# Kernel optimization log

Measured on AMD Instinct MI355X. Metric: run time of the kernel, lower is better.

The kernel has to match this reference:

```python
import jax, jax.numpy as jnp
import numpy as np

B, S, HID = 4, 2048, 1024
E, K, H = 8, 2, 8          # num_experts, topk, num_heads
DK = HID // H              # head_qk_dim = 128
DV = HID // H              # head_v_dim = 128
CAP = int(S * 1.0)         # capacity_len = int((S*K)/K * capacity)
CHUNK = 64
EPS = 1e-5


def setup_inputs() -> dict:
    key = jax.random.key(0)
    ks = jax.random.split(key, 12)
    std = 0.02  # ~ xavier_uniform with gain 2**-2.5
    return {
        "x": jax.random.normal(ks[0], (B, S, HID), jnp.float32),
        "gate_w": jax.random.normal(ks[1], (E, HID), jnp.float32) * std,
        "q_w": jax.random.normal(ks[2], (HID, HID), jnp.float32) * std,
        "k_w": jax.random.normal(ks[3], (E, HID, HID), jnp.float32) * std,
        "v_w": jax.random.normal(ks[4], (E, HID, HID), jnp.float32) * std,
        "fmq1_w": jax.random.normal(ks[5], (DK, DK), jnp.float32) * std,
        "fmq2_w": jax.random.normal(ks[6], (DK, DK), jnp.float32) * std,
        "fmk1_w": jax.random.normal(ks[7], (DK, DK), jnp.float32) * std,
        "fmk2_w": jax.random.normal(ks[8], (DK, DK), jnp.float32) * std,
        "norm_w": jnp.ones((DV,), jnp.float32),
        "o_w": jax.random.normal(ks[9], (HID, HID), jnp.float32) * std,
    }


def chunk_linear_attn(q, k, v):
    # q,k: (Bt, T, H, DK); v: (Bt, T, H, DV). Causal linear attention, chunked.
    Bt, T, Hh, Dk = q.shape
    Dv = v.shape[-1]
    nc = T // CHUNK
    q = q * (Dk ** -0.5)
    qc = q.reshape(Bt, nc, CHUNK, Hh, Dk).transpose(1, 0, 2, 3, 4)
    kc = k.reshape(Bt, nc, CHUNK, Hh, Dk).transpose(1, 0, 2, 3, 4)
    vc = v.reshape(Bt, nc, CHUNK, Hh, Dv).transpose(1, 0, 2, 3, 4)
    causal = jnp.tril(jnp.ones((CHUNK, CHUNK), q.dtype))
    def step(Sst, qkv):
        qb, kb, vb = qkv  # (Bt, CHUNK, H, D)
        attn = jnp.einsum('bihd,bjhd->bhij', qb, kb) * causal
        intra = jnp.einsum('bhij,bjhe->bihe', attn, vb)
        inter = jnp.einsum('bihd,bhde->bihe', qb, Sst)
        Sst = Sst + jnp.einsum('bjhd,bjhe->bhde', kb, vb)
        return Sst, intra + inter
    S0 = jnp.zeros((Bt, Hh, Dk, Dv), q.dtype)
    _, o = jax.lax.scan(step, S0, (qc, kc, vc))
    return o.transpose(1, 0, 2, 3, 4).reshape(Bt, T, Hh, Dv)


def _forward(x, gate_w, q_w, k_w, v_w, fmq1_w, fmq2_w, fmk1_w, fmk2_w, norm_w, o_w):
    b, s0, d = x.shape
    # ---- routing ----
    logits = jnp.einsum('bsd,ed->bse', x, gate_w)
    scores = jax.nn.softmax(logits.astype(jnp.float32), axis=-1)
    rw, sel = jax.lax.top_k(scores, K)                 # (b, s0, K)
    rw = (rw / rw.sum(-1, keepdims=True)).astype(x.dtype)
    routing_mask = jax.nn.one_hot(sel, E, dtype=jnp.int32).sum(2)  # (b, s0, E)
    # ---- transform: sort-by-(batch,expert), capacity gather ----
    s = s0 * K
    x_rep = jnp.repeat(x, K, axis=1).reshape(b * s, d)  # repeat_interleave over seq
    sel_flat = sel.reshape(b * s).astype(jnp.int32)
    batch_idx = jnp.repeat(jnp.arange(b, dtype=jnp.int32), s)
    combined = batch_idx * E + sel_flat
    sorted_indices = jnp.argsort(combined)              # stable in jax
    x_sorted = x_rep[sorted_indices]
    tokens = routing_mask.sum(axis=1)                   # (b, E) tokens per group
    flat_off = (jnp.cumsum(tokens, axis=1) + (jnp.arange(b, dtype=jnp.int32) * s)[:, None]).reshape(-1)
    starts = jnp.concatenate([jnp.zeros((1,), flat_off.dtype), flat_off[:-1]])
    idx = starts[:, None] + jnp.arange(CAP, dtype=flat_off.dtype)[None, :]
    shift = jnp.maximum(tokens.reshape(-1) - CAP, 0)    # keep last CAP tokens
    tidx = idx + shift[:, None]                         # (b*E, CAP)
    dmask = tidx < flat_off[:, None]
    tidx = jnp.where(dmask, tidx, 0)
    xe = x_sorted[tidx.reshape(-1)].reshape(b * E, CAP, d) * dmask[..., None].astype(x.dtype)
    xe = xe.reshape(b, E, CAP, d).transpose(1, 0, 2, 3)  # (E, b, CAP, d)
    # ---- projections + Hadamard feature maps ----
    q = jnp.einsum('ebtc,kc->ebtk', xe, q_w).reshape(E, b, CAP, H, DK)
    k = jnp.einsum('ebtc,ekc->ebtk', xe, k_w).reshape(E, b, CAP, H, DK)
    v = jnp.einsum('ebtc,ekc->ebtk', xe, v_w).reshape(E, b, CAP, H, DV)
    q = jnp.einsum('...d,kd->...k', q, fmq1_w) * jnp.einsum('...d,kd->...k', q, fmq2_w)
    k = jnp.einsum('...d,kd->...k', k, fmk1_w) * jnp.einsum('...d,kd->...k', k, fmk2_w)
    # ---- causal chunked linear attention per (expert, batch) slot ----
    o = chunk_linear_attn(q.reshape(E * b, CAP, H, DK),
                          k.reshape(E * b, CAP, H, DK),
                          v.reshape(E * b, CAP, H, DV))
    # ---- reconstruct: scatter-add back, undo sort, weighted topk combine ----
    oflat = o.reshape(E, b, CAP, H, DV).transpose(1, 0, 2, 3, 4).reshape(b * E * CAP, H, DV)
    oflat = oflat * dmask.reshape(-1)[:, None, None].astype(o.dtype)
    res = jnp.zeros((b * s, H, DV), o.dtype).at[tidx.reshape(-1)].add(oflat)
    inv = jnp.argsort(sorted_indices)
    restored = res[inv].reshape(b, s0, K, H, DV)
    out = (restored * rw[..., None, None]).sum(axis=2)   # (b, s0, H, DV)
    # RMSNorm over head_v_dim, merge heads, output proj
    out = out * jax.lax.rsqrt(jnp.mean(out * out, axis=-1, keepdims=True) + EPS) * norm_w
    out = out.reshape(b, s0, H * DV)
    return jnp.einsum('bsv,dv->bsd', out, o_w)


def reference(x, gate_w, q_w, k_w, v_w, fmq1_w, fmq2_w, fmk1_w, fmk2_w, norm_w, o_w):
    return _forward(x, gate_w, q_w, k_w, v_w, fmq1_w, fmq2_w, fmk1_w, fmk2_w, norm_w, o_w)
```

## Files before the change

### kernel.cpp

```cpp
#include <hip/hip_runtime.h>
#include <stdint.h>

typedef unsigned short u16;
typedef unsigned int   u32;
typedef __attribute__((ext_vector_type(4))) float f32x4;
typedef __attribute__((ext_vector_type(4))) u32   u32x4;
typedef __attribute__((ext_vector_type(8))) __bf16 bf16x8;

#define MFMA16(a,b,c) __builtin_amdgcn_mfma_f32_16x16x32_bf16((a),(b),(c),0,0,0)

#define QSCALE 0.08838834764831845f
#define RMAX   20480

__device__ __forceinline__ float bf2f(u16 x){ u32 u=((u32)x)<<16; float f; __builtin_memcpy(&f,&u,4); return f; }
__device__ __forceinline__ u16 f2bf(float f){ u32 u; __builtin_memcpy(&u,&f,4); u = u + 0x7FFFu + ((u>>16)&1u); return (u16)(u>>16); }
__device__ __forceinline__ u32 pack2(float a, float b){ return (u32)f2bf(a) | ((u32)f2bf(b)<<16); }

__device__ __forceinline__ void gl_lds(const u16* g, u16* l){
  __builtin_amdgcn_global_load_lds(
      (const __attribute__((address_space(1))) void*)g,
      (__attribute__((address_space(3))) void*)l, 16, 0, 0);
}

#define TSW(row, oct) ((row)*72 + ((((oct) ^ (((row)>>3)&7)))<<3))


__device__ __forceinline__ void cvt_body(const float* __restrict__ s, u16* __restrict__ d,
                                         long n8, int lb, int nb){
  long idx = (long)lb*256 + threadIdx.x;
  long stride = (long)nb*256;
  for (long i=idx; i<n8; i+=stride){
    const float* p = s + i*8;
    f32x4 a = *(const f32x4*)p;
    f32x4 b = *(const f32x4*)(p+4);
    u32x4 o;
    o[0]=pack2(a[0],a[1]); o[1]=pack2(a[2],a[3]); o[2]=pack2(b[0],b[1]); o[3]=pack2(b[2],b[3]);
    *(u32x4*)(d + i*8) = o;
  }
}

__device__ __forceinline__ void route_body(const float* __restrict__ x, const float* __restrict__ gw,
  int* __restrict__ sel, float* __restrict__ rw, u16* __restrict__ xb, int lb)
{
  int w = threadIdx.x>>6, lane = threadIdx.x&63;
  int tok = lb*4 + w;
  const float* xr = x + (size_t)tok*1024 + lane*16;
  f32x4 xv[4];
  #pragma unroll
  for (int q=0;q<4;q++) xv[q] = *(const f32x4*)(xr + q*4);
  {
    u16* xrow = xb + (size_t)tok*1024 + lane*16;
    u32x4 o0, o1;
    o0[0]=pack2(xv[0][0],xv[0][1]); o0[1]=pack2(xv[0][2],xv[0][3]);
    o0[2]=pack2(xv[1][0],xv[1][1]); o0[3]=pack2(xv[1][2],xv[1][3]);
    o1[0]=pack2(xv[2][0],xv[2][1]); o1[1]=pack2(xv[2][2],xv[2][3]);
    o1[2]=pack2(xv[3][0],xv[3][1]); o1[3]=pack2(xv[3][2],xv[3][3]);
    *(u32x4*)xrow     = o0;
    *(u32x4*)(xrow+8) = o1;
  }
  float part[8];
  #pragma unroll
  for (int e=0;e<8;e++){
    const float* g = gw + e*1024 + lane*16;
    float s = 0.f;
    #pragma unroll
    for (int q=0;q<4;q++){
      f32x4 gv = *(const f32x4*)(g + q*4);
      s += xv[q][0]*gv[0] + xv[q][1]*gv[1] + xv[q][2]*gv[2] + xv[q][3]*gv[3];
    }
    part[e]=s;
  }
  #pragma unroll
  for (int e=0;e<8;e++){
    float v = part[e];
    #pragma unroll
    for (int off=32; off>0; off>>=1) v += __shfl_xor(v, off, 64);
    part[e]=v;
  }
  if (lane==0){
    int i0=0; float m0=part[0];
    #pragma unroll
    for (int e=1;e<8;e++) if (part[e]>m0){ m0=part[e]; i0=e; }
    int i1=0; float m1=-3.4e38f;
    #pragma unroll
    for (int e=0;e<8;e++) if (e!=i0 && part[e]>m1){ m1=part[e]; i1=e; }
    sel[tok] = i0 | (i1<<8);
    float e1 = expf(m1-m0);
    float inv = 1.f/(1.f+e1);
    rw[tok*2+0] = inv;
    rw[tok*2+1] = e1*inv;
  }
}

__device__ __forceinline__ void prep_body(
  const float* __restrict__ q_w, const float* __restrict__ k_w,
  const float* __restrict__ fmq1, const float* __restrict__ fmq2,
  const float* __restrict__ fmk1, const float* __restrict__ fmk2,
  u16* __restrict__ wA, u16* __restrict__ wB, int l, u16* shmem)
{
  int gi = l>>3;
  int c0 = (l&7)*128;
  const float* fm; const float* ws; u16* wd;
  if (gi < 8)      { int h=gi;    fm=fmq1; ws=q_w + (size_t)h*131072; wd=wA + (size_t)h*262144; }
  else if (gi < 16){ int h=gi-8;  fm=fmq2; ws=q_w + (size_t)h*131072; wd=wA + (size_t)h*262144 + 131072; }
  else if (gi < 80){ int t=gi-16, e=t>>3, h=t&7; fm=fmk1; ws=k_w + (size_t)(e*8+h)*131072; wd=wB + (size_t)e*2097152 + (size_t)h*262144; }
  else             { int t=gi-80, e=t>>3, h=t&7; fm=fmk2; ws=k_w + (size_t)(e*8+h)*131072; wd=wB + (size_t)e*2097152 + (size_t)h*262144 + 131072; }
  u16* Af = shmem;
  u16* Bf = shmem + 128*136;
  int tid = threadIdx.x;
  for (int i=tid; i<4096; i+=256){
    int row = i>>5, col = (i&31)*4;
    f32x4 v = *(const f32x4*)&fm[row*128 + col];
    u16* dp = &Af[row*136 + col];
    *(u32*)dp     = pack2(v[0],v[1]);
    *(u32*)(dp+2) = pack2(v[2],v[3]);
  }
  for (int i=tid; i<4096; i+=256){
    int dd = i>>5, cq = (i&31)*4;
    f32x4 v = *(const f32x4*)&ws[(size_t)dd*1024 + c0 + cq];
    #pragma unroll
    for (int j=0;j<4;j++){
      int c = cq+j;
      Bf[c*136 + (dd ^ (((c>>2)&3)<<3))] = f2bf(v[j]);
    }
  }
  __syncthreads();
  int lane=tid&63, w=tid>>6, wr=w>>1, wc=w&1, lc=lane&15, lr=lane>>4;
  const f32x4 Z4 = {0.f,0.f,0.f,0.f};
  f32x4 acc[4][4];
  #pragma unroll
  for (int i=0;i<4;i++){
    #pragma unroll
    for (int j=0;j<4;j++) acc[i][j]=Z4;
  }
  #pragma unroll
  for (int kk=0; kk<4; ++kk){
    bf16x8 a[4], b[4];
    #pragma unroll
    for (int mi=0;mi<4;mi++)
      a[mi] = *(const bf16x8*)&Af[(wr*64+mi*16+lc)*136 + kk*32 + lr*8];
    #pragma unroll
    for (int ni=0;ni<4;ni++){
      int c = wc*64+ni*16+lc;
      b[ni] = *(const bf16x8*)&Bf[c*136 + ((kk*32 + lr*8) ^ (((c>>2)&3)<<3))];
    }
    #pragma unroll
    for (int mi=0;mi<4;mi++){
      #pragma unroll
      for (int ni=0;ni<4;ni++)
        acc[mi][ni] = MFMA16(a[mi], b[ni], acc[mi][ni]);
    }
  }
  int r0=lr*4;
  #pragma unroll
  for (int mi=0;mi<4;mi++){
    #pragma unroll
    for (int ni=0;ni<4;ni++){
      int col = c0 + wc*64 + ni*16 + lc;
      #pragma unroll
      for (int r=0;r<4;r++){
        int row = wr*64 + mi*16 + r0 + r;
        wd[(size_t)row*1024 + col] = f2bf(acc[mi][ni][r]);
      }
    }
  }
}

__global__ __launch_bounds__(256) void k_pre(
  const float* __restrict__ x, const float* __restrict__ gw,
  int* __restrict__ sel, float* __restrict__ rw,
  const float* __restrict__ q_w, const float* __restrict__ k_w,
  const float* __restrict__ fmq1, const float* __restrict__ fmq2,
  const float* __restrict__ fmk1, const float* __restrict__ fmk2,
  u16* __restrict__ wA, u16* __restrict__ wB, u16* __restrict__ xb,
  const float* __restrict__ v_w, u16* __restrict__ wVb)
{
  __shared__ __align__(16) u16 shmem[2*128*136];
  int bid = blockIdx.x;
  if (bid < 2048)      route_body(x, gw, sel, rw, xb, bid);
  else if (bid < 3200) prep_body(q_w, k_w, fmq1, fmq2, fmk1, fmk2, wA, wB, bid-2048, shmem);
  else                 cvt_body(v_w, wVb, 1048576L, bid-3200, 256);
}

__global__ __launch_bounds__(256) void k_cvtO(const float* __restrict__ o_w, u16* __restrict__ wOb){
  cvt_body(o_w, wOb, 131072L, blockIdx.x, 32);
}

__global__ __launch_bounds__(256) void k_count(const int* __restrict__ sel,
  int* __restrict__ slot_of, int* __restrict__ src_of, int* __restrict__ meta)
{
  int g = blockIdx.x, b = g>>3, e = g&7;
  int tid = threadIdx.x;
  __shared__ int cn[256];
  unsigned char ex[16];
  int cnt=0;
  #pragma unroll
  for (int i=0;i<16;i++){
    int t = tid*16+i;
    int sv = sel[b*2048 + (t>>1)];
    int ee = (t&1) ? ((sv>>8)&255) : (sv&255);
    ex[i]=(unsigned char)ee;
    cnt += (ee==e);
  }
  cn[tid]=cnt;
  __syncthreads();
  for (int off=1; off<256; off<<=1){
    int v = (tid>=off) ? cn[tid-off] : 0;
    __syncthreads();
    cn[tid] += v;
    __syncthreads();
  }
  int total = cn[255];
  int run = cn[tid]-cnt;
  int shift = total>2048 ? total-2048 : 0;
  #pragma unroll
  for (int i=0;i<16;i++){
    int t = tid*16+i;
    if (ex[i]==e){
      int j = run - shift;
      run++;
      slot_of[b*4096 + t] = (j>=0)? j : -1;
      if (j>=0) src_of[g*2048 + j] = t;
    }
  }
  if (tid==0) meta[g]=total;
}

__global__ void k_bases(int* meta){
  if (threadIdx.x || blockIdx.x) return;
  int basev=0, t=0;
  meta[96]=0;
  for (int g=0; g<32; ++g){
    int n = meta[g];
    int nact = n<2048 ? n : 2048;
    int npad = (nact+127)&~127;
    meta[32+g]=nact;
    meta[64+g]=npad;
    meta[129+g]=(nact+63)>>6;
    for (int i=0;i<(npad>>7);++i) meta[192+t++]=g;
    basev += npad;
    meta[97+g]=basev;
  }
  meta[161]=basev;
}

__global__ __launch_bounds__(256) void k_gather(const u16* __restrict__ xb,
  const int* __restrict__ src_of, const int* __restrict__ meta, u16* __restrict__ xg,
  int* __restrict__ tokmap)
{
  int g = blockIdx.y, jb = blockIdx.x;
  int npad = meta[64+g];
  if (jb*64 >= npad) return;
  int nact = meta[32+g], base = meta[96+g];
  int tid = threadIdx.x;
  int j = jb*64 + (tid>>2);
  int quart = tid&3;
  int src = (j<nact) ? src_of[g*2048+j] : -1;
  int token = (src>=0) ? ((g>>3)*2048 + (src>>1)) : 0;
  if (quart==0) tokmap[base+j] = token;
  u16* orow = xg + ((size_t)(base+j))*1024 + quart*256;
  if (src>=0){
    const u16* xr = xb + (size_t)token*1024 + quart*256;
    #pragma unroll
    for (int i=0;i<256;i+=8) *(u32x4*)(orow+i) = *(const u32x4*)(xr+i);
  } else {
    u32x4 z = {0,0,0,0};
    #pragma unroll
    for (int i=0;i<256;i+=8) *(u32x4*)(orow+i)=z;
  }
}

__global__ __launch_bounds__(512) void k_gemmQKV(const u16* __restrict__ xb, const u16* __restrict__ xg,
  const u16* __restrict__ wA, const u16* __restrict__ wB, const u16* __restrict__ wVb,
  u16* __restrict__ qh, u16* __restrict__ kh, u16* __restrict__ vv, const int* __restrict__ meta)
{
  int bid = blockIdx.x;
  int role, tm, tn;
  const u16 *A, *Wp; u16* outB;
  if (bid < 512){
    role=0; int l=bid, xcd=l&7, jj=l>>3, jd=jj>>3;
    tm=xcd*8+jd; tn=jj&7;
    A=xb; Wp=wA + (size_t)tn*262144; outB=qh;
  } else if (bid < 1792){
    role=1; int l=bid-512, xcd=l&7, jj=l>>3, jd=jj>>3;
    tm=xcd*20+jd; tn=jj&7;
    if (tm*128 >= meta[161]) return;
    A=xg; Wp=wB + (size_t)(meta[192+tm]&7)*2097152 + (size_t)tn*262144; outB=kh;
  } else {
    role=2; int l=bid-1792, xcd=l&7, jj=l>>3, jd=jj>>2;
    tm=xcd*20+jd; tn=jj&3;
    if (tm*128 >= meta[161]) return;
    A=xg; Wp=wVb + (size_t)(meta[192+tm]&7)*1048576 + (size_t)tn*262144; outB=vv;
  }

  __shared__ __align__(16) u16 smem[73728];

  int tid=threadIdx.x, lane=tid&63;
  int w=tid>>6, wr=w>>2, wc=w&3, lc=lane&15, lr=lane>>4;
  int swz = lc&7;
  const f32x4 Z4 = {0.f,0.f,0.f,0.f};
  f32x4 acc[4][4];
  #pragma unroll
  for(int i=0;i<4;i++){
    #pragma unroll
    for(int j2=0;j2<4;j2++) acc[i][j2]=Z4;
  }
  size_t lanoff = (size_t)(tid>>3)*1024 + (size_t)(((tid&7)^((tid>>3)&7))*8);
  const u16* Ag = A  + (size_t)tm*131072 + lanoff;
  const u16* Bg = Wp + lanoff;
  int lo = tid*8;

  #define STAGEF(ao, bo, kt) { \
    const u16* ga = Ag + (kt)*64; const u16* gb = Bg + (kt)*64; \
    gl_lds(ga,                 &smem[(ao) + lo]); \
    gl_lds(ga + (size_t)65536, &smem[(ao) + 4096 + lo]); \
    gl_lds(gb,                  &smem[(bo) + lo]); \
    gl_lds(gb + (size_t)65536,  &smem[(bo) + 4096 + lo]); \
    gl_lds(gb + (size_t)131072, &smem[(bo) + 8192 + lo]); \
    gl_lds(gb + (size_t)196608, &smem[(bo) + 12288 + lo]); }

  STAGEF(0, 24576, 0);
  STAGEF(8192, 40960, 1);
  int cur = 0;
  for (int kt=0; kt<16; ++kt){
    if (kt<15) asm volatile("s_waitcnt vmcnt(6)" ::: "memory");
    else       asm volatile("s_waitcnt vmcnt(0)" ::: "memory");
    __builtin_amdgcn_s_barrier();
    if (kt<14){
      int nid = kt+2; nid -= (nid/3)*3;
      STAGEF(nid*8192, 24576+nid*16384, kt+2);
    }
    int ao = cur*8192, bo = 24576 + cur*16384;
    __builtin_amdgcn_s_setprio(1);
    #pragma unroll
    for (int kk=0; kk<2; ++kk){
      bf16x8 a[4], b[4];
      #pragma unroll
      for (int mi=0;mi<4;mi++){
        int row = wr*64+mi*16+lc;
        a[mi] = *(const bf16x8*)&smem[ao + row*64 + (((kk*4+lr)^swz)<<3)];
      }
      #pragma unroll
      for (int ni=0;ni<4;ni++){
        int row = wc*64+ni*16+lc;
        b[ni] = *(const bf16x8*)&smem[bo + row*64 + (((kk*4+lr)^swz)<<3)];
      }
      #pragma unroll
      for (int mi=0;mi<4;mi++){
        #pragma unroll
        for (int ni=0;ni<4;ni++)
          acc[mi][ni] = MFMA16(a[mi], b[ni], acc[mi][ni]);
      }
    }
    __builtin_amdgcn_s_setprio(0);
    cur = (cur==2)?0:cur+1;
  }
  __syncthreads();
  if (role < 2){
    if (wc >= 2){
      #pragma unroll
      for (int mi=0;mi<4;mi++){
        #pragma unroll
        for (int ni=0;ni<4;ni++){
          int col = (wc-2)*64 + ni*16 + lc;
          #pragma unroll
          for (int r=0;r<4;r++)
            ((float*)smem)[(wr*64+mi*16+lr*4+r)*129 + col] = acc[mi][ni][r];
        }
      }
    }
    __syncthreads();
    if (wc < 2){
      float scl = (role==0) ? QSCALE : 1.0f;
      #pragma unroll
      for (int mi=0;mi<4;mi++){
        #pragma unroll
        for (int ni=0;ni<4;ni++){
          int col = wc*64 + ni*16 + lc;
          #pragma unroll
          for (int r=0;r<4;r++){
            int row = wr*64+mi*16+lr*4+r;
            float v = acc[mi][ni][r] * ((float*)smem)[row*129 + col] * scl;
            outB[(size_t)(tm*128+row)*1024 + tn*128 + col] = f2bf(v);
          }
        }
      }
    }
  } else {
    #pragma unroll
    for (int mi=0;mi<4;mi++){
      #pragma unroll
      for (int ni=0;ni<4;ni++){
        int col = tn*256 + wc*64 + ni*16 + lc;
        #pragma unroll
        for (int r=0;r<4;r++){
          int row = tm*128 + wr*64 + mi*16 + lr*4 + r;
          outB[(size_t)row*1024 + col] = f2bf(acc[mi][ni][r]);
        }
      }
    }
  }
  #undef STAGEF
}

__global__ __launch_bounds__(512) void k_gemmO(const u16* __restrict__ A, const u16* __restrict__ W,
  float* __restrict__ outF)
{
  int tnN = gridDim.x;
  int bid = blockIdx.y*tnN + blockIdx.x;
  int chunk = gridDim.y >> 3;
  int xcd = bid & 7, j = bid >> 3;
  int jd = j / tnN;
  int tm = xcd*chunk + jd;
  int tn = j - jd*tnN;

  __shared__ __align__(16) u16 smem[73728];

  int tid=threadIdx.x, lane=tid&63;
  int w=tid>>6, wr=w>>2, wc=w&3, lc=lane&15, lr=lane>>4;
  int swz = lc&7;
  const f32x4 Z4 = {0.f,0.f,0.f,0.f};
  f32x4 acc[4][4];
  #pragma unroll
  for(int i=0;i<4;i++){
    #pragma unroll
    for(int j2=0;j2<4;j2++) acc[i][j2]=Z4;
  }
  size_t lanoff = (size_t)(tid>>3)*1024 + (size_t)(((tid&7)^((tid>>3)&7))*8);
  const u16* Ag = A + (size_t)tm*131072 + lanoff;
  const u16* Bg = W + (size_t)tn*262144 + lanoff;
  int lo = tid*8;

  #define STAGEO(ao, bo, kt) { \
    const u16* ga = Ag + (kt)*64; const u16* gb = Bg + (kt)*64; \
    gl_lds(ga,                 &smem[(ao) + lo]); \
    gl_lds(ga + (size_t)65536, &smem[(ao) + 4096 + lo]); \
    gl_lds(gb,                  &smem[(bo) + lo]); \
    gl_lds(gb + (size_t)65536,  &smem[(bo) + 4096 + lo]); \
    gl_lds(gb + (size_t)131072, &smem[(bo) + 8192 + lo]); \
    gl_lds(gb + (size_t)196608, &smem[(bo) + 12288 + lo]); }

  STAGEO(0, 24576, 0);
  STAGEO(8192, 40960, 1);
  int cur = 0;
  for (int kt=0; kt<16; ++kt){
    if (kt<15) asm volatile("s_waitcnt vmcnt(6)" ::: "memory");
    else       asm volatile("s_waitcnt vmcnt(0)" ::: "memory");
    __builtin_amdgcn_s_barrier();
    if (kt<14){
      int nid = kt+2; nid -= (nid/3)*3;
      STAGEO(nid*8192, 24576+nid*16384, kt+2);
    }
    int ao = cur*8192, bo = 24576 + cur*16384;
    __builtin_amdgcn_s_setprio(1);
    #pragma unroll
    for (int kk=0; kk<2; ++kk){
      bf16x8 a[4], b[4];
      #pragma unroll
      for (int mi=0;mi<4;mi++){
        int row = wr*64+mi*16+lc;
        a[mi] = *(const bf16x8*)&smem[ao + row*64 + (((kk*4+lr)^swz)<<3)];
      }
      #pragma unroll
      for (int ni=0;ni<4;ni++){
        int row = wc*64+ni*16+lc;
        b[ni] = *(const bf16x8*)&smem[bo + row*64 + (((kk*4+lr)^swz)<<3)];
      }
      #pragma unroll
      for (int mi=0;mi<4;mi++){
        #pragma unroll
        for (int ni=0;ni<4;ni++)
          acc[mi][ni] = MFMA16(a[mi], b[ni], acc[mi][ni]);
      }
    }
    __builtin_amdgcn_s_setprio(0);
    cur = (cur==2)?0:cur+1;
  }
  #pragma unroll
  for (int mi=0;mi<4;mi++){
    #pragma unroll
    for (int ni=0;ni<4;ni++){
      int col = tn*256 + wc*64 + ni*16 + lc;
      #pragma unroll
      for (int r=0;r<4;r++){
        int row = tm*128 + wr*64 + mi*16 + lr*4 + r;
        outF[(size_t)row*1024 + col] = acc[mi][ni][r];
      }
    }
  }
  #undef STAGEO
}

__global__ __launch_bounds__(256,1) void k_attn(const u16* __restrict__ qv, const u16* __restrict__ kv,
  const u16* __restrict__ vv, u16* __restrict__ o, const int* __restrict__ meta,
  const int* __restrict__ tokmap)
{
  int g = blockIdx.x>>3, h = blockIdx.x&7;
  int nch = meta[129+g];
  if (nch==0) return;
  int base = meta[96+g];
  __shared__ __align__(16) u16 Qs[64*136];
  __shared__ __align__(16) u16 Ks[64*136];
  __shared__ __align__(16) u16 KTs[128*72];
  __shared__ __align__(16) u16 VTs[128*72];
  __shared__ __align__(16) u16 Ts[2*128*136];
  __shared__ __align__(16) u16 Ps[64*72];
  int tid=threadIdx.x, w=tid>>6, lane=tid&63;
  int wr=w>>1, wc=w&1;
  int lr=lane>>4, lc=lane&15;
  {
    u32x4 z={0,0,0,0};
    for (int i=tid; i<128*136/8; i+=256) *(u32x4*)&Ts[i*8]=z;
  }
  const f32x4 Z4 = {0.f,0.f,0.f,0.f};
  f32x4 accT[4][4];
  #pragma unroll
  for (int i=0;i<4;i++){
    #pragma unroll
    for (int j=0;j<4;j++) accT[i][j]=Z4;
  }
  __syncthreads();
  const u16* kb = kv + (size_t)base*1024 + h*128;
  const u16* vb = vv + (size_t)base*1024 + h*128;
  u16* ob = o + (size_t)base*1024 + h*128;
  int tso = 0;

  for (int c=0; c<nch; ++c){
    #pragma unroll
    for (int it=0; it<4; ++it){
      int id = tid + it*256;
      int row = id>>4, kc = id&15;
      int tok = tokmap[base + c*64 + row];
      *(u32x4*)&Qs[row*136 + kc*8] = *(const u32x4*)(qv + (size_t)tok*1024 + h*128 + kc*8);
      *(u32x4*)&Ks[row*136 + kc*8] = *(const u32x4*)(kb + (size_t)(c*64+row)*1024 + kc*8);
    }
    #pragma unroll
    for (int it=0; it<4; ++it){
      int id = tid + it*256;
      int j = id>>4, dg = id&15;
      int col = (((j>>3) ^ (dg&7))<<3) + (j&7);
      u32x4 kx = *(const u32x4*)(kb + (size_t)(c*64+j)*1024 + dg*8);
      u32x4 vx = *(const u32x4*)(vb + (size_t)(c*64+j)*1024 + dg*8);
      #pragma unroll
      for (int t=0;t<4;t++){
        KTs[(dg*8+t*2  )*72 + col] = (u16)(kx[t]&0xffff);
        KTs[(dg*8+t*2+1)*72 + col] = (u16)(kx[t]>>16);
        VTs[(dg*8+t*2  )*72 + col] = (u16)(vx[t]&0xffff);
        VTs[(dg*8+t*2+1)*72 + col] = (u16)(vx[t]>>16);
      }
    }
    __syncthreads();
    bf16x8 qf[2][4];
    #pragma unroll
    for (int ti=0; ti<2; ++ti){
      #pragma unroll
      for (int ks=0; ks<4; ++ks)
        qf[ti][ks] = *(const bf16x8*)&Qs[(wr*32+ti*16+lc)*136 + ks*32 + lr*8];
    }
    f32x4 accO[2][4];
    #pragma unroll
    for (int i=0;i<2;i++){
      #pragma unroll
      for (int j=0;j<4;j++) accO[i][j]=Z4;
    }
    #pragma unroll
    for (int ks=0; ks<4; ++ks){
      bf16x8 bt[4];
      #pragma unroll
      for (int te=0; te<4; ++te)
        bt[te] = *(const bf16x8*)&Ts[tso + (wc*64+te*16+lc)*136 + ks*32 + lr*8];
      #pragma unroll
      for (int ti=0; ti<2; ++ti){
        #pragma unroll
        for (int te=0; te<4; ++te)
          accO[ti][te] = MFMA16(qf[ti][ks], bt[te], accO[ti][te]);
      }
    }
    f32x4 accP[2][2];
    #pragma unroll
    for (int i=0;i<2;i++){
      #pragma unroll
      for (int j=0;j<2;j++) accP[i][j]=Z4;
    }
    #pragma unroll
    for (int ks=0; ks<4; ++ks){
      bf16x8 bk[2];
      #pragma unroll
      for (int tj=0; tj<2; ++tj)
        bk[tj] = *(const bf16x8*)&Ks[(wc*32+tj*16+lc)*136 + ks*32 + lr*8];
      #pragma unroll
      for (int ti=0; ti<2; ++ti){
        #pragma unroll
        for (int tj=0; tj<2; ++tj)
          accP[ti][tj] = MFMA16(qf[ti][ks], bk[tj], accP[ti][tj]);
      }
    }
    #pragma unroll
    for (int ti=0; ti<2; ++ti){
      #pragma unroll
      for (int tj=0; tj<2; ++tj){
        #pragma unroll
        for (int r=0;r<4;r++){
          int i = wr*32+ti*16+lr*4+r;
          int j = wc*32+tj*16+lc;
          Ps[i*72 + j] = f2bf( (j<=i) ? accP[ti][tj][r] : 0.f );
        }
      }
    }
    __syncthreads();
    #pragma unroll
    for (int ks=0; ks<2; ++ks){
      bf16x8 ap[2], bv[4];
      #pragma unroll
      for (int ti=0; ti<2; ++ti)
        ap[ti] = *(const bf16x8*)&Ps[(wr*32+ti*16+lc)*72 + ks*32 + lr*8];
      #pragma unroll
      for (int te=0; te<4; ++te)
        bv[te] = *(const bf16x8*)&VTs[TSW(wc*64+te*16+lc, ks*4+lr)];
      #pragma unroll
      for (int ti=0; ti<2; ++ti){
        #pragma unroll
        for (int te=0; te<4; ++te)
          accO[ti][te] = MFMA16(ap[ti], bv[te], accO[ti][te]);
      }
    }
    #pragma unroll
    for (int ks=0; ks<2; ++ks){
      bf16x8 av[4], bk2[4];
      #pragma unroll
      for (int te=0; te<4; ++te)
        av[te] = *(const bf16x8*)&VTs[TSW(wr*64+te*16+lc, ks*4+lr)];
      #pragma unroll
      for (int td=0; td<4; ++td)
        bk2[td] = *(const bf16x8*)&KTs[TSW(wc*64+td*16+lc, ks*4+lr)];
      #pragma unroll
      for (int te=0; te<4; ++te){
        #pragma unroll
        for (int td=0; td<4; ++td)
          accT[te][td] = MFMA16(av[te], bk2[td], accT[te][td]);
      }
    }
    int tsn = tso ^ (128*136);
    #pragma unroll
    for (int te=0; te<4; ++te){
      #pragma unroll
      for (int td=0; td<4; ++td){
        int dk = wc*64+td*16+lc;
        #pragma unroll
        for (int r=0;r<4;r++){
          int erow = wr*64+te*16+lr*4+r;
          Ts[tsn + erow*136 + dk] = f2bf(accT[te][td][r]);
        }
      }
    }
    #pragma unroll
    for (int ti=0; ti<2; ++ti){
      #pragma unroll
      for (int te=0; te<4; ++te){
        int ecol = wc*64+te*16+lc;
        #pragma unroll
        for (int r=0;r<4;r++){
          int i = wr*32+ti*16+lr*4+r;
          ob[(size_t)(c*64+i)*1024 + ecol] = f2bf(accO[ti][te][r]);
        }
      }
    }
    __syncthreads();
    tso = tsn;
  }
}

__global__ __launch_bounds__(256) void k_comb(const u16* __restrict__ o, const int* __restrict__ sel,
  const float* __restrict__ rw, const int* __restrict__ slot_of, const int* __restrict__ meta,
  const float* __restrict__ nw, u16* __restrict__ fin)
{
  int w=threadIdx.x>>6, lane=threadIdx.x&63;
  int tok = blockIdx.x*4 + w;
  int b = tok>>11;
  int sv = sel[tok];
  float acc[16];
  #pragma unroll
  for (int i=0;i<16;i++) acc[i]=0.f;
  #pragma unroll
  for (int kk=0; kk<2; ++kk){
    int e = kk ? ((sv>>8)&255) : (sv&255);
    int j = slot_of[tok*2 + kk];
    if (j < 0) continue;
    float wgt = rw[tok*2+kk];
    int row = meta[96 + b*8 + e] + j;
    const u16* orow = o + (size_t)row*1024 + lane*16;
    #pragma unroll
    for (int q=0;q<2;q++){
      u32x4 v = *(const u32x4*)(orow + q*8);
      #pragma unroll
      for (int t=0;t<4;t++){
        acc[q*8+t*2]   += wgt * bf2f((u16)(v[t]&0xffff));
        acc[q*8+t*2+1] += wgt * bf2f((u16)(v[t]>>16));
      }
    }
  }
  float ssq=0.f;
  #pragma unroll
  for (int i=0;i<16;i++) ssq += acc[i]*acc[i];
  ssq += __shfl_xor(ssq,1,64);
  ssq += __shfl_xor(ssq,2,64);
  ssq += __shfl_xor(ssq,4,64);
  float sc = rsqrtf(ssq*(1.f/128.f) + 1e-5f);
  int cbase = (lane&7)*16;
  u32x4 o0, o1;
  #pragma unroll
  for (int t=0;t<4;t++)
    o0[t] = pack2(acc[2*t]*sc*nw[cbase+2*t], acc[2*t+1]*sc*nw[cbase+2*t+1]);
  #pragma unroll
  for (int t=0;t<4;t++)
    o1[t] = pack2(acc[8+2*t]*sc*nw[cbase+8+2*t], acc[8+2*t+1]*sc*nw[cbase+8+2*t+1]);
  u16* fp = fin + (size_t)tok*1024 + lane*16;
  *(u32x4*)fp     = o0;
  *(u32x4*)(fp+8) = o1;
}

extern "C" void kernel_launch(void* const* d_in, const int* in_sizes, int n_in,
                              void* d_out, int out_size, void* d_ws, size_t ws_size,
                              hipStream_t stream)
{
  (void)in_sizes; (void)n_in;
  const float* x     = (const float*)d_in[0];
  const float* gate  = (const float*)d_in[1];
  const float* q_w   = (const float*)d_in[2];
  const float* k_w   = (const float*)d_in[3];
  const float* v_w   = (const float*)d_in[4];
  const float* fmq1  = (const float*)d_in[5];
  const float* fmq2  = (const float*)d_in[6];
  const float* fmk1  = (const float*)d_in[7];
  const float* fmk2  = (const float*)d_in[8];
  const float* norm_w= (const float*)d_in[9];
  const float* o_w   = (const float*)d_in[10];
  float* out = (float*)d_out;

  uint8_t* ws = (uint8_t*)d_ws;
  size_t off = 0;
  auto alloc = [&](size_t bytes)->void*{ void* p = ws + off; off += (bytes + 255) & ~(size_t)255; return p; };
  int*   meta = (int*)alloc(4096);
  int*   sel  = (int*)alloc(8192*4);
  float* rwb  = (float*)alloc(8192*2*4);
  int*   slot = (int*)alloc(16384*4);
  int*   srcf = (int*)alloc((size_t)32*2048*4);
  int*   tokm = (int*)alloc((size_t)RMAX*4);
  u16* wA = (u16*)alloc((size_t)2097152*2);
  u16* wB = (u16*)alloc((size_t)8*2097152*2);
  u16* xb  = (u16*)alloc((size_t)8192*1024*2);
  u16* xg  = (u16*)alloc((size_t)RMAX*1024*2);
  u16* qh  = (u16*)alloc((size_t)8192*1024*2);
  u16* kh  = (u16*)alloc((size_t)RMAX*1024*2);
  u16* vv  = (u16*)alloc((size_t)RMAX*1024*2);
  if (off > ws_size){
    hipMemsetAsync(d_out, 0x7F, (size_t)out_size*4, stream);
    return;
  }
  u16* wVb = (u16*)d_out;
  u16* ob  = xg;
  u16* fin = qh;
  u16* wOb = wA;

  k_pre<<<3456,256,0,stream>>>(x, gate, sel, rwb, q_w, k_w, fmq1, fmq2, fmk1, fmk2, wA, wB, xb, v_w, wVb);
  k_count<<<32,256,0,stream>>>(sel, slot, srcf, meta);
  k_bases<<<1,64,0,stream>>>(meta);
  k_gather<<<dim3(32,32),256,0,stream>>>(xb, srcf, meta, xg, tokm);
  k_gemmQKV<<<2432,512,0,stream>>>(xb, xg, wA, wB, wVb, qh, kh, vv, meta);
  k_cvtO<<<32,256,0,stream>>>(o_w, wOb);
  k_attn<<<256,256,0,stream>>>(qh, kh, vv, ob, meta, tokm);
  k_comb<<<2048,256,0,stream>>>(ob, sel, rwb, slot, meta, norm_w, fin);
  k_gemmO<<<dim3(4,64),512,0,stream>>>(fin, wOb, out);
}
```

Measured before the change: 416.7 us.

## Enlarge QKV GEMM M-tile to 256 rows with 4-stage K32 LDS pipeline

The fused Q/K/V GEMM now computes 256x256 (or 256x128 for the Q/K elementwise-product roles) output tiles instead of 128-row tiles. It uses a K step of 32 with a 4-deep global-to-LDS ring, a new XOR swizzle, and split barriers that interleave loads with MFMAs. Expert row groups are padded to 256 instead of 128, so the maximum row buffer and the tile-to-expert map change to match. The larger wB weight buffer moves into the output buffer and wVb moves into the workspace. The goal is higher arithmetic intensity and fewer blocks and weight reloads. The costs are more padding waste, higher register pressure from 128 accumulator floats per thread, and an occupancy hint that may force spills.

New measurement: 459.5 us. 1.1x slower.

```diff
diff --git a/kernel.cpp b/kernel.cpp
--- a/kernel.cpp
+++ b/kernel.cpp
@@ -10,7 +10,7 @@
 #define MFMA16(a,b,c) __builtin_amdgcn_mfma_f32_16x16x32_bf16((a),(b),(c),0,0,0)
 
 #define QSCALE 0.08838834764831845f
-#define RMAX   20480
+#define RMAX   24576
 
 __device__ __forceinline__ float bf2f(u16 x){ u32 u=((u32)x)<<16; float f; __builtin_memcpy(&f,&u,4); return f; }
 __device__ __forceinline__ u16 f2bf(float f){ u32 u; __builtin_memcpy(&u,&f,4); u = u + 0x7FFFu + ((u>>16)&1u); return (u16)(u>>16); }
@@ -233,11 +233,11 @@
   for (int g=0; g<32; ++g){
     int n = meta[g];
     int nact = n<2048 ? n : 2048;
-    int npad = (nact+127)&~127;
+    int npad = (nact+255)&~255;
     meta[32+g]=nact;
     meta[64+g]=npad;
     meta[129+g]=(nact+63)>>6;
-    for (int i=0;i<(npad>>7);++i) meta[192+t++]=g;
+    for (int i=0;i<(npad>>8);++i) meta[192+t++]=g;
     basev += npad;
     meta[97+g]=basev;
   }
@@ -270,102 +270,107 @@
   }
 }
 
-__global__ __launch_bounds__(512) void k_gemmQKV(const u16* __restrict__ xb, const u16* __restrict__ xg,
+__global__ __launch_bounds__(512,2) void k_gemmQKV(const u16* __restrict__ xb, const u16* __restrict__ xg,
   const u16* __restrict__ wA, const u16* __restrict__ wB, const u16* __restrict__ wVb,
   u16* __restrict__ qh, u16* __restrict__ kh, u16* __restrict__ vv, const int* __restrict__ meta)
 {
   int bid = blockIdx.x;
   int role, tm, tn;
   const u16 *A, *Wp; u16* outB;
-  if (bid < 512){
-    role=0; int l=bid, xcd=l&7, jj=l>>3, jd=jj>>3;
-    tm=xcd*8+jd; tn=jj&7;
+  if (bid < 256){
+    role=0; int l=bid, xcd=l&7, jj=l>>3;
+    int jd=jj>>3; tm=xcd*4+jd; tn=jj&7;
     A=xb; Wp=wA + (size_t)tn*262144; outB=qh;
-  } else if (bid < 1792){
-    role=1; int l=bid-512, xcd=l&7, jj=l>>3, jd=jj>>3;
-    tm=xcd*20+jd; tn=jj&7;
-    if (tm*128 >= meta[161]) return;
+  } else if (bid < 1024){
+    role=1; int l=bid-256, xcd=l&7, jj=l>>3;
+    int jd=jj>>3; tm=xcd*12+jd; tn=jj&7;
+    if (tm*256 >= meta[161]) return;
     A=xg; Wp=wB + (size_t)(meta[192+tm]&7)*2097152 + (size_t)tn*262144; outB=kh;
   } else {
-    role=2; int l=bid-1792, xcd=l&7, jj=l>>3, jd=jj>>2;
-    tm=xcd*20+jd; tn=jj&3;
-    if (tm*128 >= meta[161]) return;
+    role=2; int l=bid-1024, xcd=l&7, jj=l>>3;
+    int jd=jj>>2; tm=xcd*12+jd; tn=jj&3;
+    if (tm*256 >= meta[161]) return;
     A=xg; Wp=wVb + (size_t)(meta[192+tm]&7)*1048576 + (size_t)tn*262144; outB=vv;
   }
 
-  __shared__ __align__(16) u16 smem[73728];
+  __shared__ __align__(16) u16 smem[65536];
 
   int tid=threadIdx.x, lane=tid&63;
   int w=tid>>6, wr=w>>2, wc=w&3, lc=lane&15, lr=lane>>4;
-  int swz = lc&7;
+  int szl=(lc^(lc>>2))&3;
   const f32x4 Z4 = {0.f,0.f,0.f,0.f};
-  f32x4 acc[4][4];
-  #pragma unroll
-  for(int i=0;i<4;i++){
+  f32x4 acc[8][4];
+  #pragma unroll
+  for(int i=0;i<8;i++){
     #pragma unroll
     for(int j2=0;j2<4;j2++) acc[i][j2]=Z4;
   }
-  size_t lanoff = (size_t)(tid>>3)*1024 + (size_t)(((tid&7)^((tid>>3)&7))*8);
-  const u16* Ag = A  + (size_t)tm*131072 + lanoff;
-  const u16* Bg = Wp + lanoff;
-  int lo = tid*8;
-
-  #define STAGEF(ao, bo, kt) { \
-    const u16* ga = Ag + (kt)*64; const u16* gb = Bg + (kt)*64; \
-    gl_lds(ga,                 &smem[(ao) + lo]); \
-    gl_lds(ga + (size_t)65536, &smem[(ao) + 4096 + lo]); \
-    gl_lds(gb,                  &smem[(bo) + lo]); \
-    gl_lds(gb + (size_t)65536,  &smem[(bo) + 4096 + lo]); \
-    gl_lds(gb + (size_t)131072, &smem[(bo) + 8192 + lo]); \
-    gl_lds(gb + (size_t)196608, &smem[(bo) + 12288 + lo]); }
-
-  STAGEF(0, 24576, 0);
-  STAGEF(8192, 40960, 1);
-  int cur = 0;
-  for (int kt=0; kt<16; ++kt){
-    if (kt<15) asm volatile("s_waitcnt vmcnt(6)" ::: "memory");
-    else       asm volatile("s_waitcnt vmcnt(0)" ::: "memory");
-    __builtin_amdgcn_s_barrier();
-    if (kt<14){
-      int nid = kt+2; nid -= (nid/3)*3;
-      STAGEF(nid*8192, 24576+nid*16384, kt+2);
-    }
-    int ao = cur*8192, bo = 24576 + cur*16384;
-    __builtin_amdgcn_s_setprio(1);
-    #pragma unroll
-    for (int kk=0; kk<2; ++kk){
-      bf16x8 a[4], b[4];
-      #pragma unroll
-      for (int mi=0;mi<4;mi++){
-        int row = wr*64+mi*16+lc;
-        a[mi] = *(const bf16x8*)&smem[ao + row*64 + (((kk*4+lr)^swz)<<3)];
-      }
-      #pragma unroll
-      for (int ni=0;ni<4;ni++){
-        int row = wc*64+ni*16+lc;
-        b[ni] = *(const bf16x8*)&smem[bo + row*64 + (((kk*4+lr)^swz)<<3)];
-      }
-      #pragma unroll
-      for (int mi=0;mi<4;mi++){
-        #pragma unroll
-        for (int ni=0;ni<4;ni++)
-          acc[mi][ni] = MFMA16(a[mi], b[ni], acc[mi][ni]);
-      }
-    }
-    __builtin_amdgcn_s_setprio(0);
-    cur = (cur==2)?0:cur+1;
-  }
+  const u16* Ag = A + (size_t)tm*262144;
+  const u16* Bg = Wp;
+  int grow = tid>>2;
+  int gch  = (((tid&3)^((grow^(grow>>2))&3)))*8;
+  int lch  = (tid&3)*8;
+
+  #define STG(t_, h_) { \
+    const u16* gs = ((h_)&2) ? Bg : Ag; \
+    int rb = ((h_)&1)*128; \
+    gl_lds(gs + (size_t)(rb+grow)*1024 + (size_t)(t_)*32 + gch, \
+           smem + (((t_)&3)<<14) + (((h_)&2)?8192:0) + (rb+grow)*32 + lch); \
+  }
+
+  STG(0,0); STG(0,1); STG(0,2); STG(0,3);
+  STG(1,0); STG(1,1); STG(1,2); STG(1,3);
+  asm volatile("s_waitcnt vmcnt(4)" ::: "memory");
+  __builtin_amdgcn_s_barrier();
+
+  for (int t=0; t<32; ++t){
+    int abase=(t&3)<<14, bbase=abase+8192;
+    bf16x8 a[8];
+    #pragma unroll
+    for (int q=0;q<2;++q){
+      if (q==0){
+        #pragma unroll
+        for (int mi=0;mi<8;mi++){
+          int arow = wr*128+mi*16+lc;
+          a[mi] = *(const bf16x8*)&smem[abase + arow*32 + ((lr^szl)<<3)];
+        }
+      }
+      bf16x8 b[2];
+      #pragma unroll
+      for (int nj=0;nj<2;nj++){
+        int brow = wc*64+(q*2+nj)*16+lc;
+        b[nj] = *(const bf16x8*)&smem[bbase + brow*32 + ((lr^szl)<<3)];
+      }
+      if (t<30){ STG(t+2, q*2); STG(t+2, q*2+1); }
+      __builtin_amdgcn_s_barrier();
+      __builtin_amdgcn_s_setprio(1);
+      #pragma unroll
+      for (int mi=0;mi<8;mi++){
+        #pragma unroll
+        for (int nj=0;nj<2;nj++)
+          acc[mi][q*2+nj] = MFMA16(a[mi], b[nj], acc[mi][q*2+nj]);
+      }
+      __builtin_amdgcn_s_setprio(0);
+      if (q==1){
+        if (t<30)      asm volatile("s_waitcnt vmcnt(4)" ::: "memory");
+        else if (t==30) asm volatile("s_waitcnt vmcnt(0)" ::: "memory");
+      }
+      __builtin_amdgcn_s_barrier();
+    }
+  }
+  #undef STG
+
   __syncthreads();
   if (role < 2){
     if (wc >= 2){
       #pragma unroll
-      for (int mi=0;mi<4;mi++){
+      for (int mi=0;mi<8;mi++){
         #pragma unroll
         for (int ni=0;ni<4;ni++){
           int col = (wc-2)*64 + ni*16 + lc;
           #pragma unroll
           for (int r=0;r<4;r++)
-            ((float*)smem)[(wr*64+mi*16+lr*4+r)*129 + col] = acc[mi][ni][r];
+            ((float*)smem)[(wr*128+mi*16+lr*4+r)*128 + col] = acc[mi][ni][r];
         }
       }
     }
@@ -373,34 +378,33 @@
     if (wc < 2){
       float scl = (role==0) ? QSCALE : 1.0f;
       #pragma unroll
-      for (int mi=0;mi<4;mi++){
+      for (int mi=0;mi<8;mi++){
         #pragma unroll
         for (int ni=0;ni<4;ni++){
           int col = wc*64 + ni*16 + lc;
           #pragma unroll
           for (int r=0;r<4;r++){
-            int row = wr*64+mi*16+lr*4+r;
-            float v = acc[mi][ni][r] * ((float*)smem)[row*129 + col] * scl;
-            outB[(size_t)(tm*128+row)*1024 + tn*128 + col] = f2bf(v);
+            int row = wr*128+mi*16+lr*4+r;
+            float v = acc[mi][ni][r] * ((float*)smem)[row*128 + col] * scl;
+            outB[(size_t)(tm*256+row)*1024 + tn*128 + col] = f2bf(v);
           }
         }
       }
     }
   } else {
     #pragma unroll
-    for (int mi=0;mi<4;mi++){
+    for (int mi=0;mi<8;mi++){
       #pragma unroll
       for (int ni=0;ni<4;ni++){
         int col = tn*256 + wc*64 + ni*16 + lc;
         #pragma unroll
         for (int r=0;r<4;r++){
-          int row = tm*128 + wr*64 + mi*16 + lr*4 + r;
+          int row = tm*256 + wr*128 + mi*16 + lr*4 + r;
           outB[(size_t)row*1024 + col] = f2bf(acc[mi][ni][r]);
         }
       }
     }
   }
-  #undef STAGEF
 }
 
 __global__ __launch_bounds__(512) void k_gemmO(const u16* __restrict__ A, const u16* __restrict__ W,
@@ -746,8 +750,8 @@
   int*   slot = (int*)alloc(16384*4);
   int*   srcf = (int*)alloc((size_t)32*2048*4);
   int*   tokm = (int*)alloc((size_t)RMAX*4);
-  u16* wA = (u16*)alloc((size_t)2097152*2);
-  u16* wB = (u16*)alloc((size_t)8*2097152*2);
+  u16* wA  = (u16*)alloc((size_t)2097152*2);
+  u16* wVb = (u16*)alloc((size_t)8388608*2);
   u16* xb  = (u16*)alloc((size_t)8192*1024*2);
   u16* xg  = (u16*)alloc((size_t)RMAX*1024*2);
   u16* qh  = (u16*)alloc((size_t)8192*1024*2);
@@ -757,7 +761,7 @@
     hipMemsetAsync(d_out, 0x7F, (size_t)out_size*4, stream);
     return;
   }
-  u16* wVb = (u16*)d_out;
+  u16* wB  = (u16*)d_out;
   u16* ob  = xg;
   u16* fin = qh;
   u16* wOb = wA;
@@ -766,7 +770,7 @@
   k_count<<<32,256,0,stream>>>(sel, slot, srcf, meta);
   k_bases<<<1,64,0,stream>>>(meta);
   k_gather<<<dim3(32,32),256,0,stream>>>(xb, srcf, meta, xg, tokm);
-  k_gemmQKV<<<2432,512,0,stream>>>(xb, xg, wA, wB, wVb, qh, kh, vv, meta);
+  k_gemmQKV<<<1408,512,0,stream>>>(xb, xg, wA, wB, wVb, qh, kh, vv, meta);
   k_cvtO<<<32,256,0,stream>>>(o_w, wOb);
   k_attn<<<256,256,0,stream>>>(qh, kh, vv, ob, meta, tokm);
   k_comb<<<2048,256,0,stream>>>(ob, sel, rwb, slot, meta, norm_w, fin);
```
